# Kernel optimization log

Hardware: AMD Instinct MI355X
Metric: run time of the kernel (lower is better)

## Reference

```python
import jax, jax.numpy as jnp
import numpy as np
from jax import lax

PRED_LEN = 48  # prediction_length


def setup_inputs() -> dict:
    key = jax.random.key(0)
    ks = jax.random.split(key, 7)
    B, T, IN, H, OUT = 1024, 512, 1, 512, 1
    s = 1.0 / float(np.sqrt(H))  # PyTorch default uniform init bound
    x = jax.random.normal(ks[0], (B, T, IN), dtype=jnp.float32)
    w_ih = jax.random.uniform(ks[1], (4 * H, IN), jnp.float32, -s, s)
    w_hh = jax.random.uniform(ks[2], (4 * H, H), jnp.float32, -s, s)
    b_ih = jax.random.uniform(ks[3], (4 * H,), jnp.float32, -s, s)
    b_hh = jax.random.uniform(ks[4], (4 * H,), jnp.float32, -s, s)
    w_fc = jax.random.uniform(ks[5], (OUT, H), jnp.float32, -s, s)
    b_fc = jax.random.uniform(ks[6], (OUT,), jnp.float32, -s, s)
    return {"x": x, "w_ih": w_ih, "w_hh": w_hh, "b_ih": b_ih,
            "b_hh": b_hh, "w_fc": w_fc, "b_fc": b_fc}


def _lstm_cell(xt, h, c, w_ih, w_hh, b):
    # PyTorch gate order: input, forget, cell(g), output
    g = xt @ w_ih.T + h @ w_hh.T + b  # [B, 4H]
    i, f, gg, o = jnp.split(g, 4, axis=-1)
    c = jax.nn.sigmoid(f) * c + jax.nn.sigmoid(i) * jnp.tanh(gg)
    h = jax.nn.sigmoid(o) * jnp.tanh(c)
    return h, c


def reference(x, w_ih, w_hh, b_ih, b_hh, w_fc, b_fc):
    B = x.shape[0]
    H = w_hh.shape[1]
    b = b_ih + b_hh
    h0 = jnp.zeros((B, H), x.dtype)
    c0 = jnp.zeros((B, H), x.dtype)

    # --- encoder: full-sequence LSTM over x, batch_first -> scan over time ---
    def enc_step(carry, xt):
        h, c = carry
        h, c = _lstm_cell(xt, h, c, w_ih, w_hh, b)
        return (h, c), None

    (h, c), _ = lax.scan(enc_step, (h0, c0), jnp.swapaxes(x, 0, 1))

    def dec_step(carry, _):
        h, c = carry
        out = h @ w_fc.T + b_fc  # dropout is identity at inference
        h, c = _lstm_cell(out, h, c, w_ih, w_hh, b)
        return (h, c), out

    _, preds = lax.scan(dec_step, (h, c), None, length=PRED_LEN)  # [P, B, OUT]
    return jnp.swapaxes(preds, 0, 1)  # [B, P, OUT]
```

## Files before the change

kernel.cpp:

```cpp
#include <hip/hip_runtime.h>

typedef _Float16 f16x8 __attribute__((ext_vector_type(8)));
typedef float    f32x4 __attribute__((ext_vector_type(4)));
typedef unsigned long long u64;
typedef u64 u64x2 __attribute__((ext_vector_type(2)));

constexpr int BATCH = 1024;
constexpr int HDIM  = 512;
constexpr int TENC  = 512;
constexpr int PRED  = 48;
constexpr int STEPS = TENC + PRED - 1;
constexpr int NG    = 64;
constexpr int GB    = 16;
constexpr int UBU   = 64;
constexpr int HB_OFF = 32768;

constexpr u64 TAG_MASK = 0x0001000100010001ull;
__device__ __forceinline__ u64 tag_of(int t) {
  return ((u64)(t & 1) | ((u64)((t >> 1) & 1) << 16)) * 0x0000000100000001ull;
}

__global__ void init_kernel(int* wsi) {
  int idx = blockIdx.x * blockDim.x + threadIdx.x;
  int stride = gridDim.x * blockDim.x;
  const int nws = (HB_OFF + BATCH * HDIM * 2) / 4;
  for (int i = idx; i < nws; i += stride) wsi[i] = 0;
}

static __device__ __forceinline__ f16x8 load16_llc(const _Float16* p) {
  f16x8 v;
  asm volatile("global_load_dwordx4 %0, %1, off sc0 sc1"
               : "=v"(v) : "v"((u64)p) : "memory");
  return v;
}
static __device__ __forceinline__ unsigned loadc_llc(const void* p) {
  unsigned v;
  asm volatile("global_load_dword %0, %1, off sc0 sc1"
               : "=v"(v) : "v"((u64)p) : "memory");
  return v;
}
static __device__ __forceinline__ float loadx(const float* p) {
  float v;
  asm volatile("global_load_dword %0, %1, off"
               : "=v"(v) : "v"((u64)p) : "memory");
  return v;
}
static __device__ __forceinline__ void sleep_bk(int stage) {
  if (stage == 0)      __builtin_amdgcn_s_sleep(1);
  else if (stage == 1) __builtin_amdgcn_s_sleep(2);
  else if (stage == 2) __builtin_amdgcn_s_sleep(4);
  else                 __builtin_amdgcn_s_sleep(8);
}
static __device__ __forceinline__ void wait_vm0_fenced() {
  asm volatile("s_waitcnt vmcnt(0)" ::: "memory");
  __builtin_amdgcn_sched_barrier(0);
}
static __device__ __forceinline__ void wait_vm1_fenced() {
  asm volatile("s_waitcnt vmcnt(1)" ::: "memory");
  __builtin_amdgcn_sched_barrier(0);
}
static __device__ __forceinline__ void lds_barrier() {
  asm volatile("s_waitcnt lgkmcnt(0)" ::: "memory");
  __builtin_amdgcn_s_barrier();
}

__global__ __launch_bounds__(256, 1) void lstm_persist(
    const float* __restrict__ x,
    const float* __restrict__ w_ih,
    const float* __restrict__ w_hh,
    const float* __restrict__ b_ih,
    const float* __restrict__ b_hh,
    const float* __restrict__ w_fc,
    const float* __restrict__ b_fc,
    float* __restrict__ out,
    _Float16* __restrict__ hbuf)
{
  const int bid  = blockIdx.x;
  const int gA   = bid >> 3;
  const int ub   = bid & 7;
  const int tid  = threadIdx.x;
  const int wid  = tid >> 6;
  const int lane = tid & 63;
  const int quad = lane >> 4;
  const int lcol = lane & 15;
  const int bA0  = gA * GB;
  const int bB0  = bA0 + NG / 2 * GB;
  const int myu  = ub * UBU + wid * 16 + lcol;

  __shared__ __align__(16) _Float16 hsA[GB][520];
  __shared__ __align__(16) _Float16 hsB[GB][520];
  __shared__ __align__(16) _Float16 wz[520];
  __shared__ __align__(16) _Float16 rp[GB][UBU];

  for (int k = tid; k < 512; k += 256) wz[k] = (_Float16)w_fc[k];
  if (tid < 8) wz[512 + tid] = (_Float16)0.f;

  f16x8 wf[4][16];
  float wih[4], bias[4];
#pragma unroll
  for (int nt = 0; nt < 4; ++nt) {
    const int j = nt * HDIM + myu;
    wih[nt]  = w_ih[j];
    bias[nt] = b_ih[j] + b_hh[j];
#pragma unroll
    for (int kc = 0; kc < 16; ++kc) {
      const float* s = w_hh + (size_t)j * HDIM + kc * 32 + quad * 8;
      f16x8 v;
#pragma unroll
      for (int i = 0; i < 8; ++i) v[i] = (_Float16)s[i];
      wf[nt][kc] = v;
    }
  }
  const float bfc = b_fc[0];

  float cstA[4], cstB[4];
#pragma unroll
  for (int r = 0; r < 4; ++r) { cstA[r] = 0.f; cstB[r] = 0.f; }

  f16x8 tA[4], tB[4];
  float xA[4], xB[4];

  auto issue4 = [&](f16x8* tr, const _Float16* base) {
#pragma unroll
    for (int i = 0; i < 4; ++i) {
      const int c = i * 256 + tid;
      tr[i] = load16_llc(base + (size_t)(c >> 6) * HDIM + (c & 63) * 8);
    }
  };
  auto validate4 = [&](f16x8* tr, const _Float16* base, u64 expect) {
    const unsigned exp32 = (unsigned)expect & 0x00010001u;
    unsigned stale = 0;
#pragma unroll
    for (int i = 0; i < 4; ++i) {
      u64x2 w2 = __builtin_bit_cast(u64x2, tr[i]);
      if (((w2[0] & TAG_MASK) != expect) || ((w2[1] & TAG_MASK) != expect))
        stale |= 1u << i;
    }
    int slp = 0;
    while (stale) {
      sleep_bk(slp);
      if (slp < 3) ++slp;
      unsigned cv[4];
#pragma unroll
      for (int i = 0; i < 4; ++i)
        if (stale & (1u << i)) {
          const int c = i * 256 + tid;
          cv[i] = loadc_llc(base + (size_t)(c >> 6) * HDIM + (c & 63) * 8);
        }
      wait_vm0_fenced();
      unsigned rdy = 0;
#pragma unroll
      for (int i = 0; i < 4; ++i)
        if ((stale & (1u << i)) && ((cv[i] & 0x00010001u) == exp32))
          rdy |= 1u << i;
      if (!rdy) continue;
#pragma unroll
      for (int i = 0; i < 4; ++i)
        if (rdy & (1u << i)) {
          const int c = i * 256 + tid;
          tr[i] = load16_llc(base + (size_t)(c >> 6) * HDIM + (c & 63) * 8);
        }
      wait_vm0_fenced();
#pragma unroll
      for (int i = 0; i < 4; ++i)
        if (rdy & (1u << i)) {
          u64x2 w2 = __builtin_bit_cast(u64x2, tr[i]);
          if (((w2[0] & TAG_MASK) == expect) && ((w2[1] & TAG_MASK) == expect))
            stale &= ~(1u << i);
        }
    }
  };
  auto stage4 = [&](f16x8* tr, _Float16 (*hsp)[520]) {
#pragma unroll
    for (int i = 0; i < 4; ++i) {
      const int c = i * 256 + tid;
      *reinterpret_cast<f16x8*>(&hsp[c >> 6][(c & 63) * 8]) = tr[i];
    }
  };
  auto gemm = [&](const _Float16 (*hsp)[520], f32x4* acc, f32x4& accF, bool dec) {
#pragma unroll
    for (int kc = 0; kc < 16; ++kc) {
      const f16x8 a = *reinterpret_cast<const f16x8*>(&hsp[lcol][kc * 32 + quad * 8]);
#pragma unroll
      for (int nt = 0; nt < 4; ++nt)
        acc[nt] = __builtin_amdgcn_mfma_f32_16x16x32_f16(a, wf[nt][kc], acc[nt], 0, 0, 0);
      if (dec) {
        const f16x8 wv = *reinterpret_cast<const f16x8*>(
            &wz[(lcol == 0) ? (kc * 32 + quad * 8) : 512]);
        accF = __builtin_amdgcn_mfma_f32_16x16x32_f16(a, wv, accF, 0, 0, 0);
      }
    }
  };
  auto tail = [&](f32x4* acc, f32x4& accF, float* xv, float* cstv,
                  int bX0, int t, _Float16* hnxt, bool dec) {
    if (dec) {
#pragma unroll
      for (int r = 0; r < 4; ++r) xv[r] = __shfl(accF[r], quad * 16) + bfc;
      if (ub == 0 && wid == 0 && lcol == 0) {
        const int p = t - TENC;
#pragma unroll
        for (int r = 0; r < 4; ++r)
          out[(size_t)(bX0 + quad * 4 + r) * PRED + p] = accF[r] + bfc;
      }
    }
    if (t < STEPS) {
      const u64 tagnew = tag_of(t + 1);
#pragma unroll
      for (int r = 0; r < 4; ++r) {
        const float xt = xv[r];
        const float gi = acc[0][r] + xt * wih[0] + bias[0];
        const float gf = acc[1][r] + xt * wih[1] + bias[1];
        const float gg = acc[2][r] + xt * wih[2] + bias[2];
        const float go = acc[3][r] + xt * wih[3] + bias[3];
        const float si = 1.f / (1.f + __expf(-gi));
        const float sf = 1.f / (1.f + __expf(-gf));
        const float so = 1.f / (1.f + __expf(-go));
        const float tg = 1.f - 2.f / (1.f + __expf(2.f * gg));
        const float cn = sf * cstv[r] + si * tg;
        cstv[r] = cn;
        const float tc = 1.f - 2.f / (1.f + __expf(2.f * cn));
        rp[quad * 4 + r][wid * 16 + lcol] = (_Float16)(so * tc);
      }
      lds_barrier();
      const u64 hv = *reinterpret_cast<const u64*>(&rp[tid >> 4][(tid & 15) * 4]);
      const u64 p4 = (hv & ~TAG_MASK) | tagnew;
      _Float16* dst = hnxt + (size_t)(bX0 + (tid >> 4)) * HDIM
                      + ub * UBU + (tid & 15) * 4;
      __hip_atomic_store((u64*)dst, p4, __ATOMIC_RELAXED,
                         __HIP_MEMORY_SCOPE_AGENT);
    }
  };

  issue4(tA, hbuf + (size_t)bA0 * HDIM);
#pragma unroll
  for (int r = 0; r < 4; ++r)
    xA[r] = loadx(x + (size_t)(bA0 + quad * 4 + r) * TENC + 0);

  for (int t = 0; t <= STEPS; ++t) {
    const _Float16* hcur = hbuf + (size_t)(t & 1) * BATCH * HDIM;
    _Float16*       hnxt = hbuf + (size_t)((t + 1) & 1) * BATCH * HDIM;
    const u64 expect = tag_of(t);
    const bool dec = (t >= TENC);

    if (t == 0) wait_vm0_fenced();
    else        wait_vm1_fenced();
    validate4(tA, hcur + (size_t)bA0 * HDIM, expect);
    stage4(tA, hsA);
    lds_barrier();
    issue4(tB, hcur + (size_t)bB0 * HDIM);
    if (!dec) {
#pragma unroll
      for (int r = 0; r < 4; ++r)
        xB[r] = loadx(x + (size_t)(bB0 + quad * 4 + r) * TENC + t);
    }

    f32x4 accA[4], accFA;
#pragma unroll
    for (int nt = 0; nt < 4; ++nt) accA[nt] = (f32x4){0.f, 0.f, 0.f, 0.f};
    accFA = (f32x4){0.f, 0.f, 0.f, 0.f};
    gemm(hsA, accA, accFA, dec);
    tail(accA, accFA, xA, cstA, bA0, t, hnxt, dec);

    wait_vm1_fenced();
    validate4(tB, hcur + (size_t)bB0 * HDIM, expect);
    stage4(tB, hsB);
    lds_barrier();
    if (t < STEPS)
      issue4(tA, hnxt + (size_t)bA0 * HDIM);
    if (t + 1 < TENC) {
#pragma unroll
      for (int r = 0; r < 4; ++r)
        xA[r] = loadx(x + (size_t)(bA0 + quad * 4 + r) * TENC + t + 1);
    }

    f32x4 accB[4], accFB;
#pragma unroll
    for (int nt = 0; nt < 4; ++nt) accB[nt] = (f32x4){0.f, 0.f, 0.f, 0.f};
    accFB = (f32x4){0.f, 0.f, 0.f, 0.f};
    gemm(hsB, accB, accFB, dec);
    tail(accB, accFB, xB, cstB, bB0, t, hnxt, dec);
  }
}

extern "C" void kernel_launch(void* const* d_in, const int* in_sizes, int n_in,
                              void* d_out, int out_size, void* d_ws, size_t ws_size,
                              hipStream_t stream) {
  const float* x    = (const float*)d_in[0];
  const float* w_ih = (const float*)d_in[1];
  const float* w_hh = (const float*)d_in[2];
  const float* b_ih = (const float*)d_in[3];
  const float* b_hh = (const float*)d_in[4];
  const float* w_fc = (const float*)d_in[5];
  const float* b_fc = (const float*)d_in[6];
  float* out = (float*)d_out;
  _Float16* hbuf = (_Float16*)((char*)d_ws + HB_OFF);

  hipLaunchKernelGGL(init_kernel, dim3(256), dim3(256), 0, stream, (int*)d_ws);
  hipLaunchKernelGGL(lstm_persist, dim3(256), dim3(256), 0, stream,
                     x, w_ih, w_hh, b_ih, b_hh, w_fc, b_fc, out, hbuf);
}
```

Before: 2.956 ms.

## Halve grid to 128 blocks, each pipelining four batch groups per step

```diff
diff --git a/kernel.cpp b/kernel.cpp
--- a/kernel.cpp
+++ b/kernel.cpp
@@ -10,9 +10,10 @@
 constexpr int TENC  = 512;
 constexpr int PRED  = 48;
 constexpr int STEPS = TENC + PRED - 1;
-constexpr int NG    = 64;
 constexpr int GB    = 16;
 constexpr int UBU   = 64;
+constexpr int GPB   = 4;
+constexpr int NCL   = 16;
 constexpr int HB_OFF = 32768;
 
 constexpr u64 TAG_MASK = 0x0001000100010001ull;
@@ -55,8 +56,16 @@
   asm volatile("s_waitcnt vmcnt(0)" ::: "memory");
   __builtin_amdgcn_sched_barrier(0);
 }
-static __device__ __forceinline__ void wait_vm1_fenced() {
-  asm volatile("s_waitcnt vmcnt(1)" ::: "memory");
+static __device__ __forceinline__ void wait_vm8_fenced() {
+  asm volatile("s_waitcnt vmcnt(8)" ::: "memory");
+  __builtin_amdgcn_sched_barrier(0);
+}
+static __device__ __forceinline__ void wait_vm9_fenced() {
+  asm volatile("s_waitcnt vmcnt(9)" ::: "memory");
+  __builtin_amdgcn_sched_barrier(0);
+}
+static __device__ __forceinline__ void wait_vm10_fenced() {
+  asm volatile("s_waitcnt vmcnt(10)" ::: "memory");
   __builtin_amdgcn_sched_barrier(0);
 }
 static __device__ __forceinline__ void lds_barrier() {
@@ -76,21 +85,20 @@
     _Float16* __restrict__ hbuf)
 {
   const int bid  = blockIdx.x;
-  const int gA   = bid >> 3;
+  const int cl   = bid >> 3;
   const int ub   = bid & 7;
   const int tid  = threadIdx.x;
   const int wid  = tid >> 6;
   const int lane = tid & 63;
   const int quad = lane >> 4;
   const int lcol = lane & 15;
-  const int bA0  = gA * GB;
-  const int bB0  = bA0 + NG / 2 * GB;
   const int myu  = ub * UBU + wid * 16 + lcol;
 
   __shared__ __align__(16) _Float16 hsA[GB][520];
   __shared__ __align__(16) _Float16 hsB[GB][520];
   __shared__ __align__(16) _Float16 wz[520];
   __shared__ __align__(16) _Float16 rp[GB][UBU];
+  __shared__ float outs[GPB][GB][PRED];
 
   for (int k = tid; k < 512; k += 256) wz[k] = (_Float16)w_fc[k];
   if (tid < 8) wz[512 + tid] = (_Float16)0.f;
@@ -113,12 +121,14 @@
   }
   const float bfc = b_fc[0];
 
-  float cstA[4], cstB[4];
-#pragma unroll
-  for (int r = 0; r < 4; ++r) { cstA[r] = 0.f; cstB[r] = 0.f; }
-
-  f16x8 tA[4], tB[4];
-  float xA[4], xB[4];
+  float cst[GPB][4];
+#pragma unroll
+  for (int g = 0; g < GPB; ++g)
+#pragma unroll
+    for (int r = 0; r < 4; ++r) cst[g][r] = 0.f;
+
+  f16x8 tXa[4], tXb[4];
+  float xva[4], xvb[4];
 
   auto issue4 = [&](f16x8* tr, const _Float16* base) {
 #pragma unroll
@@ -191,50 +201,21 @@
       }
     }
   };
-  auto tail = [&](f32x4* acc, f32x4& accF, float* xv, float* cstv,
-                  int bX0, int t, _Float16* hnxt, bool dec) {
-    if (dec) {
-#pragma unroll
-      for (int r = 0; r < 4; ++r) xv[r] = __shfl(accF[r], quad * 16) + bfc;
-      if (ub == 0 && wid == 0 && lcol == 0) {
-        const int p = t - TENC;
-#pragma unroll
-        for (int r = 0; r < 4; ++r)
-          out[(size_t)(bX0 + quad * 4 + r) * PRED + p] = accF[r] + bfc;
-      }
-    }
-    if (t < STEPS) {
-      const u64 tagnew = tag_of(t + 1);
-#pragma unroll
-      for (int r = 0; r < 4; ++r) {
-        const float xt = xv[r];
-        const float gi = acc[0][r] + xt * wih[0] + bias[0];
-        const float gf = acc[1][r] + xt * wih[1] + bias[1];
-        const float gg = acc[2][r] + xt * wih[2] + bias[2];
-        const float go = acc[3][r] + xt * wih[3] + bias[3];
-        const float si = 1.f / (1.f + __expf(-gi));
-        const float sf = 1.f / (1.f + __expf(-gf));
-        const float so = 1.f / (1.f + __expf(-go));
-        const float tg = 1.f - 2.f / (1.f + __expf(2.f * gg));
-        const float cn = sf * cstv[r] + si * tg;
-        cstv[r] = cn;
-        const float tc = 1.f - 2.f / (1.f + __expf(2.f * cn));
-        rp[quad * 4 + r][wid * 16 + lcol] = (_Float16)(so * tc);
-      }
-      lds_barrier();
-      const u64 hv = *reinterpret_cast<const u64*>(&rp[tid >> 4][(tid & 15) * 4]);
-      const u64 p4 = (hv & ~TAG_MASK) | tagnew;
-      _Float16* dst = hnxt + (size_t)(bX0 + (tid >> 4)) * HDIM
-                      + ub * UBU + (tid & 15) * 4;
-      __hip_atomic_store((u64*)dst, p4, __ATOMIC_RELAXED,
-                         __HIP_MEMORY_SCOPE_AGENT);
-    }
-  };
-
-  issue4(tA, hbuf + (size_t)bA0 * HDIM);
-#pragma unroll
-  for (int r = 0; r < 4; ++r)
-    xA[r] = loadx(x + (size_t)(bA0 + quad * 4 + r) * TENC + 0);
+
+  lds_barrier();
+
+  {
+    const int b0 = cl * GB;
+    issue4(tXa, hbuf + (size_t)b0 * HDIM);
+#pragma unroll
+    for (int r = 0; r < 4; ++r)
+      xva[r] = loadx(x + (size_t)(b0 + quad * 4 + r) * TENC);
+    const int b1 = (cl + NCL) * GB;
+    issue4(tXb, hbuf + (size_t)b1 * HDIM);
+#pragma unroll
+    for (int r = 0; r < 4; ++r)
+      xvb[r] = loadx(x + (size_t)(b1 + quad * 4 + r) * TENC);
+  }
 
   for (int t = 0; t <= STEPS; ++t) {
     const _Float16* hcur = hbuf + (size_t)(t & 1) * BATCH * HDIM;
@@ -242,43 +223,108 @@
     const u64 expect = tag_of(t);
     const bool dec = (t >= TENC);
 
-    if (t == 0) wait_vm0_fenced();
-    else        wait_vm1_fenced();
-    validate4(tA, hcur + (size_t)bA0 * HDIM, expect);
-    stage4(tA, hsA);
-    lds_barrier();
-    issue4(tB, hcur + (size_t)bB0 * HDIM);
-    if (!dec) {
-#pragma unroll
-      for (int r = 0; r < 4; ++r)
-        xB[r] = loadx(x + (size_t)(bB0 + quad * 4 + r) * TENC + t);
-    }
-
-    f32x4 accA[4], accFA;
-#pragma unroll
-    for (int nt = 0; nt < 4; ++nt) accA[nt] = (f32x4){0.f, 0.f, 0.f, 0.f};
-    accFA = (f32x4){0.f, 0.f, 0.f, 0.f};
-    gemm(hsA, accA, accFA, dec);
-    tail(accA, accFA, xA, cstA, bA0, t, hnxt, dec);
-
-    wait_vm1_fenced();
-    validate4(tB, hcur + (size_t)bB0 * HDIM, expect);
-    stage4(tB, hsB);
-    lds_barrier();
-    if (t < STEPS)
-      issue4(tA, hnxt + (size_t)bA0 * HDIM);
-    if (t + 1 < TENC) {
-#pragma unroll
-      for (int r = 0; r < 4; ++r)
-        xA[r] = loadx(x + (size_t)(bA0 + quad * 4 + r) * TENC + t + 1);
-    }
-
-    f32x4 accB[4], accFB;
-#pragma unroll
-    for (int nt = 0; nt < 4; ++nt) accB[nt] = (f32x4){0.f, 0.f, 0.f, 0.f};
-    accFB = (f32x4){0.f, 0.f, 0.f, 0.f};
-    gemm(hsB, accB, accFB, dec);
-    tail(accB, accFB, xB, cstB, bB0, t, hnxt, dec);
+#pragma unroll
+    for (int g = 0; g < GPB; ++g) {
+      const int bG0 = (cl + NCL * g) * GB;
+      f16x8* tcur = (g & 1) ? tXb : tXa;
+      float* xcur = (g & 1) ? xvb : xva;
+      _Float16 (*hsp)[520] = (g & 1) ? hsB : hsA;
+
+      if (t == 0) {
+        if (g == 0)      wait_vm8_fenced();
+        else if (g == 1) wait_vm9_fenced();
+        else             wait_vm10_fenced();
+      } else if (t == STEPS) {
+        if (g == 0)      wait_vm10_fenced();
+        else if (g == 1) wait_vm9_fenced();
+        else if (g == 2) wait_vm8_fenced();
+        else             wait_vm0_fenced();
+      } else {
+        wait_vm10_fenced();
+      }
+      asm volatile("" :: "v"(xcur[0]), "v"(xcur[1]),
+                         "v"(xcur[2]), "v"(xcur[3]));
+
+      validate4(tcur, hcur + (size_t)bG0 * HDIM, expect);
+      stage4(tcur, hsp);
+      lds_barrier();
+
+      f32x4 acc[4], accF;
+#pragma unroll
+      for (int nt = 0; nt < 4; ++nt) acc[nt] = (f32x4){0.f, 0.f, 0.f, 0.f};
+      accF = (f32x4){0.f, 0.f, 0.f, 0.f};
+      gemm(hsp, acc, accF, dec);
+
+      float xcell[4];
+      if (dec) {
+#pragma unroll
+        for (int r = 0; r < 4; ++r) xcell[r] = __shfl(accF[r], quad * 16) + bfc;
+        if (ub == 0 && wid == 0 && lcol == 0) {
+          const int p = t - TENC;
+#pragma unroll
+          for (int r = 0; r < 4; ++r)
+            outs[g][quad * 4 + r][p] = accF[r] + bfc;
+        }
+      } else {
+#pragma unroll
+        for (int r = 0; r < 4; ++r) xcell[r] = xcur[r];
+      }
+
+      const int gp  = (g + 2) & 3;
+      const int bP0 = (cl + NCL * gp) * GB;
+      f16x8* tpre = (gp & 1) ? tXb : tXa;
+      float* xpre = (gp & 1) ? xvb : xva;
+
+      if (t < STEPS) {
+        const u64 tagnew = tag_of(t + 1);
+#pragma unroll
+        for (int r = 0; r < 4; ++r) {
+          const float xt = xcell[r];
+          const float gi = acc[0][r] + xt * wih[0] + bias[0];
+          const float gf = acc[1][r] + xt * wih[1] + bias[1];
+          const float gg = acc[2][r] + xt * wih[2] + bias[2];
+          const float go = acc[3][r] + xt * wih[3] + bias[3];
+          const float si = 1.f / (1.f + __expf(-gi));
+          const float sf = 1.f / (1.f + __expf(-gf));
+          const float so = 1.f / (1.f + __expf(-go));
+          const float tg = 1.f - 2.f / (1.f + __expf(2.f * gg));
+          const float cn = sf * cst[g][r] + si * tg;
+          cst[g][r] = cn;
+          const float tc = 1.f - 2.f / (1.f + __expf(2.f * cn));
+          rp[quad * 4 + r][wid * 16 + lcol] = (_Float16)(so * tc);
+        }
+        lds_barrier();
+        const u64 hv = *reinterpret_cast<const u64*>(&rp[tid >> 4][(tid & 15) * 4]);
+        const u64 p4 = (hv & ~TAG_MASK) | tagnew;
+        const _Float16* ptgt = (g < 2) ? (hcur + (size_t)bP0 * HDIM)
+                                       : (hnxt + (size_t)bP0 * HDIM);
+        issue4(tpre, ptgt);
+        const int xi = (g < 2) ? t : (t + 1);
+        const int xc = (xi < TENC) ? xi : (TENC - 1);
+#pragma unroll
+        for (int r = 0; r < 4; ++r)
+          xpre[r] = loadx(x + (size_t)(bP0 + quad * 4 + r) * TENC + xc);
+        _Float16* dst = hnxt + (size_t)(bG0 + (tid >> 4)) * HDIM
+                        + ub * UBU + (tid & 15) * 4;
+        __hip_atomic_store((u64*)dst, p4, __ATOMIC_RELAXED,
+                           __HIP_MEMORY_SCOPE_AGENT);
+      } else if (g < 2) {
+        issue4(tpre, hcur + (size_t)bP0 * HDIM);
+#pragma unroll
+        for (int r = 0; r < 4; ++r)
+          xpre[r] = loadx(x + (size_t)(bP0 + quad * 4 + r) * TENC + (TENC - 1));
+      }
+    }
+  }
+
+  lds_barrier();
+  if (ub == 0) {
+    for (int k = tid; k < GPB * GB * PRED; k += 256) {
+      const int g  = k / (GB * PRED);
+      const int rm = k % (GB * PRED);
+      out[(size_t)((cl + NCL * g) * GB + rm / PRED) * PRED + (rm % PRED)] =
+          outs[g][rm / PRED][rm % PRED];
+    }
   }
 }
 
@@ -296,6 +342,6 @@
   _Float16* hbuf = (_Float16*)((char*)d_ws + HB_OFF);
 
   hipLaunchKernelGGL(init_kernel, dim3(256), dim3(256), 0, stream, (int*)d_ws);
-  hipLaunchKernelGGL(lstm_persist, dim3(256), dim3(256), 0, stream,
+  hipLaunchKernelGGL(lstm_persist, dim3(128), dim3(256), 0, stream,
                      x, w_ih, w_hh, b_ih, b_hh, w_fc, b_fc, out, hbuf);
 }
```

After: 5.132 ms. +73.6%, slower.

## Split gate GEMM across 8 waves and redistribute LSTM epilogue via LDS

Applied to the files above, without the earlier changes.

```diff
diff --git a/kernel.cpp b/kernel.cpp
--- a/kernel.cpp
+++ b/kernel.cpp
@@ -64,7 +64,7 @@
   __builtin_amdgcn_s_barrier();
 }
 
-__global__ __launch_bounds__(256, 1) void lstm_persist(
+__global__ __launch_bounds__(512, 2) void lstm_persist(
     const float* __restrict__ x,
     const float* __restrict__ w_ih,
     const float* __restrict__ w_hh,
@@ -80,58 +80,67 @@
   const int ub   = bid & 7;
   const int tid  = threadIdx.x;
   const int wid  = tid >> 6;
+  const int ws   = wid >> 2;
+  const int wq   = wid & 3;
   const int lane = tid & 63;
   const int quad = lane >> 4;
   const int lcol = lane & 15;
   const int bA0  = gA * GB;
   const int bB0  = bA0 + NG / 2 * GB;
-  const int myu  = ub * UBU + wid * 16 + lcol;
+  const int myu  = ub * UBU + wq * 16 + lcol;
+  const int cb   = tid >> 5;
+  const int cu   = (tid * 2) & 63;
 
   __shared__ __align__(16) _Float16 hsA[GB][520];
   __shared__ __align__(16) _Float16 hsB[GB][520];
   __shared__ __align__(16) _Float16 wz[520];
-  __shared__ __align__(16) _Float16 rp[GB][UBU];
-
-  for (int k = tid; k < 512; k += 256) wz[k] = (_Float16)w_fc[k];
+  __shared__ float gl[4][GB][68];
+  __shared__ float xls[GB];
+  __shared__ float outs[2][GB][PRED];
+
+  wz[tid < 512 ? tid : 0] = (_Float16)w_fc[tid < 512 ? tid : 0];
   if (tid < 8) wz[512 + tid] = (_Float16)0.f;
 
-  f16x8 wf[4][16];
-  float wih[4], bias[4];
-#pragma unroll
-  for (int nt = 0; nt < 4; ++nt) {
-    const int j = nt * HDIM + myu;
-    wih[nt]  = w_ih[j];
-    bias[nt] = b_ih[j] + b_hh[j];
+  f16x8 wf2[2][16];
+#pragma unroll
+  for (int ntl = 0; ntl < 2; ++ntl) {
+    const int j = (2 * ws + ntl) * HDIM + myu;
 #pragma unroll
     for (int kc = 0; kc < 16; ++kc) {
       const float* s = w_hh + (size_t)j * HDIM + kc * 32 + quad * 8;
       f16x8 v;
 #pragma unroll
       for (int i = 0; i < 8; ++i) v[i] = (_Float16)s[i];
-      wf[nt][kc] = v;
+      wf2[ntl][kc] = v;
     }
   }
+  float wihc[2][4], biasc[2][4];
+#pragma unroll
+  for (int e = 0; e < 2; ++e)
+#pragma unroll
+    for (int g = 0; g < 4; ++g) {
+      const int j = g * HDIM + ub * UBU + cu + e;
+      wihc[e][g]  = w_ih[j];
+      biasc[e][g] = b_ih[j] + b_hh[j];
+    }
   const float bfc = b_fc[0];
 
-  float cstA[4], cstB[4];
-#pragma unroll
-  for (int r = 0; r < 4; ++r) { cstA[r] = 0.f; cstB[r] = 0.f; }
-
-  f16x8 tA[4], tB[4];
-  float xA[4], xB[4];
-
-  auto issue4 = [&](f16x8* tr, const _Float16* base) {
-#pragma unroll
-    for (int i = 0; i < 4; ++i) {
-      const int c = i * 256 + tid;
+  float cstA2[2] = {0.f, 0.f}, cstB2[2] = {0.f, 0.f};
+  f16x8 tA[2], tB[2];
+  float xA, xB;
+
+  auto issue2 = [&](f16x8* tr, const _Float16* base) {
+#pragma unroll
+    for (int i = 0; i < 2; ++i) {
+      const int c = i * 512 + tid;
       tr[i] = load16_llc(base + (size_t)(c >> 6) * HDIM + (c & 63) * 8);
     }
   };
-  auto validate4 = [&](f16x8* tr, const _Float16* base, u64 expect) {
+  auto validate2 = [&](f16x8* tr, const _Float16* base, u64 expect) {
     const unsigned exp32 = (unsigned)expect & 0x00010001u;
     unsigned stale = 0;
 #pragma unroll
-    for (int i = 0; i < 4; ++i) {
+    for (int i = 0; i < 2; ++i) {
       u64x2 w2 = __builtin_bit_cast(u64x2, tr[i]);
       if (((w2[0] & TAG_MASK) != expect) || ((w2[1] & TAG_MASK) != expect))
         stale |= 1u << i;
@@ -140,29 +149,29 @@
     while (stale) {
       sleep_bk(slp);
       if (slp < 3) ++slp;
-      unsigned cv[4];
-#pragma unroll
-      for (int i = 0; i < 4; ++i)
+      unsigned cv[2];
+#pragma unroll
+      for (int i = 0; i < 2; ++i)
         if (stale & (1u << i)) {
-          const int c = i * 256 + tid;
+          const int c = i * 512 + tid;
           cv[i] = loadc_llc(base + (size_t)(c >> 6) * HDIM + (c & 63) * 8);
         }
       wait_vm0_fenced();
       unsigned rdy = 0;
 #pragma unroll
-      for (int i = 0; i < 4; ++i)
+      for (int i = 0; i < 2; ++i)
         if ((stale & (1u << i)) && ((cv[i] & 0x00010001u) == exp32))
           rdy |= 1u << i;
       if (!rdy) continue;
 #pragma unroll
-      for (int i = 0; i < 4; ++i)
+      for (int i = 0; i < 2; ++i)
         if (rdy & (1u << i)) {
-          const int c = i * 256 + tid;
+          const int c = i * 512 + tid;
           tr[i] = load16_llc(base + (size_t)(c >> 6) * HDIM + (c & 63) * 8);
         }
       wait_vm0_fenced();
 #pragma unroll
-      for (int i = 0; i < 4; ++i)
+      for (int i = 0; i < 2; ++i)
         if (rdy & (1u << i)) {
           u64x2 w2 = __builtin_bit_cast(u64x2, tr[i]);
           if (((w2[0] & TAG_MASK) == expect) && ((w2[1] & TAG_MASK) == expect))
@@ -170,71 +179,73 @@
         }
     }
   };
-  auto stage4 = [&](f16x8* tr, _Float16 (*hsp)[520]) {
-#pragma unroll
-    for (int i = 0; i < 4; ++i) {
-      const int c = i * 256 + tid;
+  auto stage2 = [&](f16x8* tr, _Float16 (*hsp)[520]) {
+#pragma unroll
+    for (int i = 0; i < 2; ++i) {
+      const int c = i * 512 + tid;
       *reinterpret_cast<f16x8*>(&hsp[c >> 6][(c & 63) * 8]) = tr[i];
     }
   };
-  auto gemm = [&](const _Float16 (*hsp)[520], f32x4* acc, f32x4& accF, bool dec) {
+  auto gemm2 = [&](const _Float16 (*hsp)[520], f32x4* acc, f32x4& accF, bool dec) {
 #pragma unroll
     for (int kc = 0; kc < 16; ++kc) {
       const f16x8 a = *reinterpret_cast<const f16x8*>(&hsp[lcol][kc * 32 + quad * 8]);
-#pragma unroll
-      for (int nt = 0; nt < 4; ++nt)
-        acc[nt] = __builtin_amdgcn_mfma_f32_16x16x32_f16(a, wf[nt][kc], acc[nt], 0, 0, 0);
-      if (dec) {
+      acc[0] = __builtin_amdgcn_mfma_f32_16x16x32_f16(a, wf2[0][kc], acc[0], 0, 0, 0);
+      acc[1] = __builtin_amdgcn_mfma_f32_16x16x32_f16(a, wf2[1][kc], acc[1], 0, 0, 0);
+      if (dec && ws == 0) {
         const f16x8 wv = *reinterpret_cast<const f16x8*>(
             &wz[(lcol == 0) ? (kc * 32 + quad * 8) : 512]);
         accF = __builtin_amdgcn_mfma_f32_16x16x32_f16(a, wv, accF, 0, 0, 0);
       }
     }
   };
-  auto tail = [&](f32x4* acc, f32x4& accF, float* xv, float* cstv,
-                  int bX0, int t, _Float16* hnxt, bool dec) {
-    if (dec) {
-#pragma unroll
-      for (int r = 0; r < 4; ++r) xv[r] = __shfl(accF[r], quad * 16) + bfc;
-      if (ub == 0 && wid == 0 && lcol == 0) {
-        const int p = t - TENC;
-#pragma unroll
-        for (int r = 0; r < 4; ++r)
-          out[(size_t)(bX0 + quad * 4 + r) * PRED + p] = accF[r] + bfc;
-      }
-    }
+  auto phase_epi = [&](f32x4* acc, f32x4& accF, float xreg, float* cstv,
+                       int bX0, int gidx, int t, _Float16* hnxt, bool dec) {
+#pragma unroll
+    for (int ntl = 0; ntl < 2; ++ntl)
+#pragma unroll
+      for (int r = 0; r < 4; ++r)
+        gl[2 * ws + ntl][quad * 4 + r][wq * 16 + lcol] = acc[ntl][r];
+    if (dec && wid == 0 && lcol == 0) {
+#pragma unroll
+      for (int r = 0; r < 4; ++r) xls[quad * 4 + r] = accF[r] + bfc;
+    }
+    lds_barrier();
+    if (dec && ub == 0 && (tid & 31) == 0)
+      outs[gidx][cb][t - TENC] = xls[cb];
+    const float xt = dec ? xls[cb] : xreg;
     if (t < STEPS) {
-      const u64 tagnew = tag_of(t + 1);
-#pragma unroll
-      for (int r = 0; r < 4; ++r) {
-        const float xt = xv[r];
-        const float gi = acc[0][r] + xt * wih[0] + bias[0];
-        const float gf = acc[1][r] + xt * wih[1] + bias[1];
-        const float gg = acc[2][r] + xt * wih[2] + bias[2];
-        const float go = acc[3][r] + xt * wih[3] + bias[3];
+      const unsigned tag32 = (unsigned)tag_of(t + 1);
+      unsigned v32 = 0;
+#pragma unroll
+      for (int e = 0; e < 2; ++e) {
+        const int u = cu + e;
+        const float gi = gl[0][cb][u] + xt * wihc[e][0] + biasc[e][0];
+        const float gf = gl[1][cb][u] + xt * wihc[e][1] + biasc[e][1];
+        const float gg = gl[2][cb][u] + xt * wihc[e][2] + biasc[e][2];
+        const float go = gl[3][cb][u] + xt * wihc[e][3] + biasc[e][3];
         const float si = 1.f / (1.f + __expf(-gi));
         const float sf = 1.f / (1.f + __expf(-gf));
         const float so = 1.f / (1.f + __expf(-go));
         const float tg = 1.f - 2.f / (1.f + __expf(2.f * gg));
-        const float cn = sf * cstv[r] + si * tg;
-        cstv[r] = cn;
+        const float cn = sf * cstv[e] + si * tg;
+        cstv[e] = cn;
         const float tc = 1.f - 2.f / (1.f + __expf(2.f * cn));
-        rp[quad * 4 + r][wid * 16 + lcol] = (_Float16)(so * tc);
+        const unsigned short hb =
+            __builtin_bit_cast(unsigned short, (_Float16)(so * tc));
+        v32 |= ((unsigned)hb) << (16 * e);
       }
-      lds_barrier();
-      const u64 hv = *reinterpret_cast<const u64*>(&rp[tid >> 4][(tid & 15) * 4]);
-      const u64 p4 = (hv & ~TAG_MASK) | tagnew;
-      _Float16* dst = hnxt + (size_t)(bX0 + (tid >> 4)) * HDIM
-                      + ub * UBU + (tid & 15) * 4;
-      __hip_atomic_store((u64*)dst, p4, __ATOMIC_RELAXED,
-                         __HIP_MEMORY_SCOPE_AGENT);
-    }
-  };
-
-  issue4(tA, hbuf + (size_t)bA0 * HDIM);
-#pragma unroll
-  for (int r = 0; r < 4; ++r)
-    xA[r] = loadx(x + (size_t)(bA0 + quad * 4 + r) * TENC + 0);
+      v32 = (v32 & ~0x00010001u) | tag32;
+      unsigned* dst = (unsigned*)(hnxt + (size_t)(bX0 + cb) * HDIM
+                                  + ub * UBU + cu);
+      __hip_atomic_store(dst, v32, __ATOMIC_RELAXED, __HIP_MEMORY_SCOPE_AGENT);
+    }
+  };
+
+  lds_barrier();
+
+  issue2(tA, hbuf + (size_t)bA0 * HDIM);
+  xA = loadx(x + (size_t)(bA0 + cb) * TENC + 0);
 
   for (int t = 0; t <= STEPS; ++t) {
     const _Float16* hcur = hbuf + (size_t)(t & 1) * BATCH * HDIM;
@@ -244,41 +255,48 @@
 
     if (t == 0) wait_vm0_fenced();
     else        wait_vm1_fenced();
-    validate4(tA, hcur + (size_t)bA0 * HDIM, expect);
-    stage4(tA, hsA);
+    asm volatile("" :: "v"(xA));
+    validate2(tA, hcur + (size_t)bA0 * HDIM, expect);
+    stage2(tA, hsA);
     lds_barrier();
-    issue4(tB, hcur + (size_t)bB0 * HDIM);
-    if (!dec) {
-#pragma unroll
-      for (int r = 0; r < 4; ++r)
-        xB[r] = loadx(x + (size_t)(bB0 + quad * 4 + r) * TENC + t);
-    }
-
-    f32x4 accA[4], accFA;
-#pragma unroll
-    for (int nt = 0; nt < 4; ++nt) accA[nt] = (f32x4){0.f, 0.f, 0.f, 0.f};
+    issue2(tB, hcur + (size_t)bB0 * HDIM);
+    xB = loadx(x + (size_t)(bB0 + cb) * TENC + (t < TENC ? t : TENC - 1));
+
+    f32x4 accA[2], accFA;
+    accA[0] = (f32x4){0.f, 0.f, 0.f, 0.f};
+    accA[1] = (f32x4){0.f, 0.f, 0.f, 0.f};
     accFA = (f32x4){0.f, 0.f, 0.f, 0.f};
-    gemm(hsA, accA, accFA, dec);
-    tail(accA, accFA, xA, cstA, bA0, t, hnxt, dec);
-
-    wait_vm1_fenced();
-    validate4(tB, hcur + (size_t)bB0 * HDIM, expect);
-    stage4(tB, hsB);
+    gemm2(hsA, accA, accFA, dec);
+    phase_epi(accA, accFA, xA, cstA2, bA0, 0, t, hnxt, dec);
+
+    if (t == STEPS) wait_vm0_fenced();
+    else            wait_vm1_fenced();
+    asm volatile("" :: "v"(xB));
+    validate2(tB, hcur + (size_t)bB0 * HDIM, expect);
+    stage2(tB, hsB);
     lds_barrier();
-    if (t < STEPS)
-      issue4(tA, hnxt + (size_t)bA0 * HDIM);
-    if (t + 1 < TENC) {
-#pragma unroll
-      for (int r = 0; r < 4; ++r)
-        xA[r] = loadx(x + (size_t)(bA0 + quad * 4 + r) * TENC + t + 1);
-    }
-
-    f32x4 accB[4], accFB;
-#pragma unroll
-    for (int nt = 0; nt < 4; ++nt) accB[nt] = (f32x4){0.f, 0.f, 0.f, 0.f};
+    if (t < STEPS) {
+      issue2(tA, hnxt + (size_t)bA0 * HDIM);
+      xA = loadx(x + (size_t)(bA0 + cb) * TENC
+                 + (t + 1 < TENC ? t + 1 : TENC - 1));
+    }
+
+    f32x4 accB[2], accFB;
+    accB[0] = (f32x4){0.f, 0.f, 0.f, 0.f};
+    accB[1] = (f32x4){0.f, 0.f, 0.f, 0.f};
     accFB = (f32x4){0.f, 0.f, 0.f, 0.f};
-    gemm(hsB, accB, accFB, dec);
-    tail(accB, accFB, xB, cstB, bB0, t, hnxt, dec);
+    gemm2(hsB, accB, accFB, dec);
+    phase_epi(accB, accFB, xB, cstB2, bB0, 1, t, hnxt, dec);
+  }
+
+  lds_barrier();
+  if (ub == 0) {
+    for (int k = tid; k < 2 * GB * PRED; k += 512) {
+      const int g  = k / (GB * PRED);
+      const int rm = k % (GB * PRED);
+      out[(size_t)((g ? bB0 : bA0) + rm / PRED) * PRED + (rm % PRED)] =
+          outs[g][rm / PRED][rm % PRED];
+    }
   }
 }
 
@@ -296,6 +314,6 @@
   _Float16* hbuf = (_Float16*)((char*)d_ws + HB_OFF);
 
   hipLaunchKernelGGL(init_kernel, dim3(256), dim3(256), 0, stream, (int*)d_ws);
-  hipLaunchKernelGGL(lstm_persist, dim3(256), dim3(256), 0, stream,
+  hipLaunchKernelGGL(lstm_persist, dim3(256), dim3(512), 0, stream,
                      x, w_ih, w_hh, b_ih, b_hh, w_fc, b_fc, out, hbuf);
 }
```

Result: faster. 2.652 ms (-10.3%).
